# Kernel tuning notes

Hardware: AMD Instinct MI355X
Metric: run time of the kernel (lower is better)

Reference implementation:

```python
import jax, jax.numpy as jnp
import numpy as np

N = 50000          # nodes
E = 400000         # edges (before self loops)
F_IN = 128         # NUM_FEATURES
HID = 32           # hidden_dim
H = 12             # heads
HC = H * HID       # concat dim = 384
CLASSES = 40       # NUM_CLASSES
NEG_SLOPE = 0.2    # PyG GATv2 default


def setup_inputs() -> dict:
    key = jax.random.key(0)
    ks = jax.random.split(key, 16)

    def p(k, shape, fan_in):
        return (jax.random.normal(k, shape, jnp.float32) / np.sqrt(fan_in)).astype(jnp.float32)

    return {
        "x": jax.random.normal(ks[0], (N, F_IN), jnp.float32),
        "edge_index": jax.random.randint(ks[1], (2, E), 0, N, jnp.int32),
        # GATv2 layer 1 (share_weights=False)
        "Wl1": p(ks[2], (F_IN, HC), F_IN),
        "Wr1": p(ks[3], (F_IN, HC), F_IN),
        "a1": p(ks[4], (H, HID), HID),
        "b1": jnp.zeros((HC,), jnp.float32),
        # GATv2 layer 2
        "Wl2": p(ks[5], (HC, HC), HC),
        "Wr2": p(ks[6], (HC, HC), HC),
        "a2": p(ks[7], (H, HID), HID),
        "b2": jnp.zeros((HC,), jnp.float32),
        # MLP head
        "W3": p(ks[8], (HC, HID), HC),
        "b3": jnp.zeros((HID,), jnp.float32),
        "W4": p(ks[9], (HID, CLASSES), HID),
        "b4": jnp.zeros((CLASSES,), jnp.float32),
    }


def _gatv2(x, Wl, Wr, att, bias, src, dst):
    # source/target linear projections, per-head
    xl = (x @ Wl).reshape(-1, H, HID)   # [N,H,C] (message features)
    xr = (x @ Wr).reshape(-1, H, HID)   # [N,H,C]
    # per-edge attention logits: a^T LeakyReLU(xl_src + xr_dst)
    e = jax.nn.leaky_relu(xl[src] + xr[dst], NEG_SLOPE)   # [E',H,C]
    logit = jnp.einsum('ehc,hc->eh', e, att)              # [E',H]
    # segment softmax over incoming edges per dst node (self loops guarantee nonempty)
    m = jax.ops.segment_max(logit, dst, num_segments=N)   # [N,H]
    ex = jnp.exp(logit - m[dst])
    denom = jax.ops.segment_sum(ex, dst, num_segments=N)  # [N,H]
    alpha = ex / denom[dst]                                # [E',H]
    # weighted scatter-add of source messages
    out = jax.ops.segment_sum(xl[src] * alpha[:, :, None], dst, num_segments=N)
    return out.reshape(-1, HC) + bias


def reference(x, edge_index, Wl1, Wr1, a1, b1, Wl2, Wr2, a2, b2, W3, b3, W4, b4):
    # add_self_loops=True (PyG default)
    loops = jnp.arange(N, dtype=edge_index.dtype)
    src = jnp.concatenate([edge_index[0], loops])
    dst = jnp.concatenate([edge_index[1], loops])
    # dropout p=0.6 is identity in eval mode
    h = _gatv2(x, Wl1, Wr1, a1, b1, src, dst)
    h = jax.nn.elu(h)
    h = _gatv2(h, Wl2, Wr2, a2, b2, src, dst)
    h = jax.nn.elu(h)
    h = jax.nn.elu(h @ W3 + b3)
    h = h @ W4 + b4
    return jax.nn.log_softmax(h, axis=1)
```

## Files before the change

kernel.cpp:

```cpp
#include <hip/hip_runtime.h>
#include <hip/hip_bf16.h>
#include <math.h>

#define N_NODES 50000
#define E_EDGES 400000
#define EN_TOT  (E_EDGES + N_NODES)
#define F_IN    128
#define HC      384
#define CLASSES 40

typedef short short8 __attribute__((ext_vector_type(8)));
typedef float floatx4 __attribute__((ext_vector_type(4)));
typedef float floatx2 __attribute__((ext_vector_type(2)));
typedef unsigned int uint;

struct u3 { uint x, y, z; };

__device__ __forceinline__ float bf2f(unsigned short u) {
  union { unsigned int i; float f; } x; x.i = ((unsigned int)u) << 16; return x.f;
}
__device__ __forceinline__ unsigned short f2bf(float f) {
  union { float f; unsigned int i; } x; x.f = f;
  unsigned int r = x.i + 0x7fffu + ((x.i >> 16) & 1u);
  return (unsigned short)(r >> 16);
}
__device__ __forceinline__ float fin(float v) {
  return (fabsf(v) < 1e30f) ? v : 0.f;
}
__device__ __forceinline__ float rdw(const void* p, int idx, int fp32) {
  return fp32 ? ((const float*)p)[idx] : bf2f(((const unsigned short*)p)[idx]);
}

#if __has_builtin(__builtin_amdgcn_exp2f)
#define EXP2F(x) __builtin_amdgcn_exp2f(x)
#else
#define EXP2F(x) exp2f(x)
#endif

#if __has_builtin(__builtin_amdgcn_update_dpp)
#define DPP_ADD(w, ctrl) \
  (w += __int_as_float(__builtin_amdgcn_update_dpp(0, __float_as_int(w), ctrl, 0xf, 0xf, true)))
#define REDUCE16(w) do { DPP_ADD(w, 0xB1); DPP_ADD(w, 0x4E); DPP_ADD(w, 0x141); DPP_ADD(w, 0x140); } while (0)
#else
#define REDUCE16(w) do { w += __shfl_xor(w, 1); w += __shfl_xor(w, 2); \
                         w += __shfl_xor(w, 4); w += __shfl_xor(w, 8); } while (0)
#endif

__global__ void k_sentinel(float* out, int n) {
  int i = blockIdx.x * 256 + threadIdx.x;
  if (i < n) out[i] = 111.0f;
}

__global__ void k_detect_zero(const unsigned short* __restrict__ x, int* __restrict__ flag,
                              int* __restrict__ counts, int* __restrict__ cursor) {
  int i = blockIdx.x * 256 + threadIdx.x;
  if (i < N_NODES) { counts[i] = 0; cursor[i] = 0; }
  if (blockIdx.x == 0 && threadIdx.x < 64) {
    int L = threadIdx.x;
    int sane = 0;
#pragma unroll
    for (int t = 0; t < 4; ++t) {
      unsigned short u = x[(size_t)(L * 4 + t) * 2];
      unsigned int mag = u & 0x7FFFu;
      unsigned int e   = (u >> 7) & 0xFFu;
      if (mag == 0u || (e >= 96u && e <= 159u)) sane++;
    }
    sane += __shfl_xor(sane, 1);
    sane += __shfl_xor(sane, 2);
    sane += __shfl_xor(sane, 4);
    sane += __shfl_xor(sane, 8);
    sane += __shfl_xor(sane, 16);
    sane += __shfl_xor(sane, 32);
    if (L == 0) flag[0] = (sane < 179) ? 1 : 0;
  }
}

__global__ void k_cvt(const void* __restrict__ x, unsigned short* __restrict__ Xb,
                      const int* __restrict__ flagp) {
  int i = blockIdx.x * 256 + threadIdx.x;
  if (i >= N_NODES * F_IN / 8) return;
  if (flagp[0]) {
    const floatx4* p = (const floatx4*)x + (size_t)i * 2;
    floatx4 f0 = p[0], f1 = p[1];
    short8 o;
#pragma unroll
    for (int j = 0; j < 4; ++j) { o[j] = (short)f2bf(f0[j]); o[4 + j] = (short)f2bf(f1[j]); }
    ((short8*)Xb)[i] = o;
  } else {
    ((short8*)Xb)[i] = ((const short8*)x)[i];
  }
}

__global__ void k_count(const int* __restrict__ ei, int* __restrict__ counts) {
  int e = blockIdx.x * 256 + threadIdx.x;
  if (e >= EN_TOT) return;
  int dst = (e < E_EDGES) ? ei[E_EDGES + e] : (e - E_EDGES);
  if ((unsigned)dst < N_NODES) atomicAdd(&counts[dst], 1);
}

__global__ void k_scan1(const int* __restrict__ counts, int* __restrict__ row_start,
                        int* __restrict__ bsum) {
  int b = blockIdx.x, tid = threadIdx.x;
  int i = b * 1024 + tid;
  int v = (i < N_NODES) ? counts[i] : 0;
  int lane = tid & 63, w = tid >> 6;
  int x = v;
#pragma unroll
  for (int d = 1; d < 64; d <<= 1) { int t = __shfl_up(x, d); if (lane >= d) x += t; }
  __shared__ int wsum[16];
  if (lane == 63) wsum[w] = x;
  __syncthreads();
  if (w == 0) {
    int y = (lane < 16) ? wsum[lane] : 0;
#pragma unroll
    for (int d = 1; d < 16; d <<= 1) { int t = __shfl_up(y, d); if (lane >= d) y += t; }
    if (lane < 16) wsum[lane] = y;
  }
  __syncthreads();
  if (w > 0) x += wsum[w - 1];
  if (i < N_NODES) row_start[i + 1] = x;
  if (tid == 1023) bsum[b] = x;
}

__global__ void k_scan23(int* __restrict__ row_start, const int* __restrict__ bsum, int nb) {
  int b = blockIdx.x, tid = threadIdx.x;
  __shared__ int sadd;
  if (tid < 64) {
    int lane = tid;
    int x = (lane < nb) ? bsum[lane] : 0;
#pragma unroll
    for (int d = 1; d < 64; d <<= 1) { int t = __shfl_up(x, d); if (lane >= d) x += t; }
    int pre = __shfl(x, (b > 0) ? (b - 1) : 0);
    if (tid == 0) sadd = (b > 0) ? pre : 0;
  }
  __syncthreads();
  int add = sadd;
  int i = b * 1024 + tid;
  if (i < N_NODES) row_start[i + 1] += add;
  if (i == 0) row_start[0] = 0;
}

__global__ void k_fill(const int* __restrict__ ei, const int* __restrict__ row_start,
                       int* __restrict__ cursor, int* __restrict__ csr_src) {
  int e = blockIdx.x * 256 + threadIdx.x;
  if (e >= EN_TOT) return;
  int src, dst;
  if (e < E_EDGES) { src = ei[e]; dst = ei[E_EDGES + e]; }
  else             { src = dst = e - E_EDGES; }
  if ((unsigned)dst >= N_NODES) return;
  int pos = atomicAdd(&cursor[dst], 1);
  int slot = row_start[dst] + pos;
  if ((unsigned)slot < EN_TOT) csr_src[slot] = src;
}

#define PK_J1 (F_IN * HC)
#define PK_J2 (2 * PK_J1)
#define PK_J3 (PK_J2 + HC * HC)
#define PK_J4 (PK_J3 + HC * HC)
#define PK_J5 (PK_J4 + HC * 32)
__global__ void k_pack_all(const void* __restrict__ Wl1, const void* __restrict__ Wr1,
                           const void* __restrict__ Wl2, const void* __restrict__ Wr2,
                           const void* __restrict__ W3,
                           unsigned short* __restrict__ BpL1, unsigned short* __restrict__ BpR1,
                           unsigned short* __restrict__ BpL2, unsigned short* __restrict__ BpR2,
                           unsigned short* __restrict__ Bp3, const int* __restrict__ flagp) {
  int gid = blockIdx.x * 256 + threadIdx.x;
  if (gid >= PK_J5) return;
  int fp32 = flagp[0];
  const void* src; unsigned short* dst; int NT, idx;
  if (gid < PK_J2)      { NT = 24; if (gid < PK_J1) { src = Wl1; dst = BpL1; idx = gid; }
                                   else             { src = Wr1; dst = BpR1; idx = gid - PK_J1; } }
  else if (gid < PK_J4) { NT = 24; if (gid < PK_J3) { src = Wl2; dst = BpL2; idx = gid - PK_J2; }
                                   else             { src = Wr2; dst = BpR2; idx = gid - PK_J3; } }
  else                  { NT = 2;  src = W3; dst = Bp3; idx = gid - PK_J4; }
  int N  = NT * 16;
  int j  = idx & 7;
  int L  = (idx >> 3) & 63;
  int t  = idx >> 9;
  int nt = t % NT;
  int kt = t / NT;
  int k  = kt * 32 + ((L >> 4) * 8) + j;
  int n  = nt * 16 + (L & 15);
  float v = rdw(src, k * N + n, fp32);
  dst[idx] = f2bf(fin(v));
}

#define LOADB(dst, kt) do { _Pragma("unroll") for (int n = 0; n < 6; ++n) \
    dst[n] = ((const short8*)Bp)[((size_t)((kt) * 24 + nt0 + n)) * 64 + lane]; } while (0)
#define DOMFMA(bf, kt) do { \
    short8 af[4]; \
    _Pragma("unroll") for (int mf = 0; mf < 4; ++mf) { \
      int row = mf * 16 + rsel; \
      int col = (kt) * 64 + kk16 * 16; \
      af[mf] = *(const short8*)(smem + row * RS + (col ^ ((row & 7) << 4))); } \
    _Pragma("unroll") for (int n = 0; n < 6; ++n) \
      _Pragma("unroll") for (int mf = 0; mf < 4; ++mf) \
        acc[mf][n] = __builtin_amdgcn_mfma_f32_16x16x32_bf16(af[mf], bf[n], acc[mf][n], 0, 0, 0); } while (0)

template<int NK>
__global__ __launch_bounds__(256, 2) void k_gemm2(const unsigned short* __restrict__ A_,
                       const unsigned short* __restrict__ BpL,
                       const unsigned short* __restrict__ BpR,
                       unsigned short* __restrict__ CL, unsigned short* __restrict__ CR) {
  constexpr int RS = NK * 64;
  __shared__ __align__(16) char smem[64 * 776];
  int which = blockIdx.x & 1;
  int bt    = blockIdx.x >> 1;
  const unsigned short* Bp = which ? BpR : BpL;
  unsigned short* C        = which ? CR  : CL;
  int tid  = threadIdx.x;
  int wave = tid >> 6, lane = tid & 63;
  int m0   = bt * 64;

  {
    uint4 v[NK];
#pragma unroll
    for (int i = 0; i < NK; ++i) {
      int o   = (i * 256 + tid) * 16;
      int row = o / RS;
      int rem = o - row * RS;
      int rg  = m0 + row; if (rg >= N_NODES) rg = N_NODES - 1;
      v[i] = *(const uint4*)((const char*)A_ + (size_t)rg * RS + rem);
    }
#pragma unroll
    for (int i = 0; i < NK; ++i) {
      int o   = (i * 256 + tid) * 16;
      int row = o / RS;
      int rem = o - row * RS;
      *(uint4*)(smem + row * RS + (rem ^ ((row & 7) << 4))) = v[i];
    }
  }

  int nt0  = wave * 6;
  int kk16 = (lane >> 4);
  int rsel = lane & 15;
  floatx4 acc[4][6];
#pragma unroll
  for (int mf = 0; mf < 4; ++mf)
#pragma unroll
    for (int n = 0; n < 6; ++n) acc[mf][n] = (floatx4){0.f, 0.f, 0.f, 0.f};

  short8 b0[6], b1[6], b2[6];
  LOADB(b0, 0);
  LOADB(b1, 1);
  __syncthreads();

#pragma unroll
  for (int kt = 0; kt < NK; ++kt) {
    if (kt + 2 < NK) {
      if (((kt + 2) % 3) == 0)      LOADB(b0, kt + 2);
      else if (((kt + 2) % 3) == 1) LOADB(b1, kt + 2);
      else                          LOADB(b2, kt + 2);
    }
    if ((kt % 3) == 0)      DOMFMA(b0, kt);
    else if ((kt % 3) == 1) DOMFMA(b1, kt);
    else                    DOMFMA(b2, kt);
  }

  __syncthreads();
  int qr = lane >> 4, ccol = lane & 15;
#pragma unroll
  for (int n = 0; n < 6; ++n) {
    int col = (nt0 + n) * 16 + ccol;
#pragma unroll
    for (int mf = 0; mf < 4; ++mf)
#pragma unroll
      for (int r = 0; r < 4; ++r) {
        int row = mf * 16 + qr * 4 + r;
        *(unsigned short*)(smem + row * 776 + col * 2) = f2bf(fin(acc[mf][n][r]));
      }
  }
  __syncthreads();
#pragma unroll
  for (int j = 0; j < 16; ++j) {
    int row = wave * 16 + j;
    int rg  = m0 + row;
    if (rg < N_NODES) {
      u3 val = *(const u3*)(smem + row * 776 + lane * 12);
      *(u3*)((char*)C + (size_t)rg * 768 + lane * 12) = val;
    }
  }
}

__global__ void k_mlp1_mfma(const unsigned short* __restrict__ H2,
                            const unsigned short* __restrict__ Bp3,
                            const void* __restrict__ b3, float* __restrict__ H3,
                            const int* __restrict__ flagp) {
  int fp32 = flagp[0];
  int lane = threadIdx.x;
  int m0   = blockIdx.x * 16;
  int row  = m0 + (lane & 15);
  int kk   = (lane >> 4) * 8;
  floatx4 acc[2];
  acc[0] = (floatx4){0.f, 0.f, 0.f, 0.f};
  acc[1] = (floatx4){0.f, 0.f, 0.f, 0.f};
#pragma unroll
  for (int kt = 0; kt < 12; ++kt) {
    short8 af = *(const short8*)(H2 + (size_t)row * HC + kt * 32 + kk);
    const short8* bp = (const short8*)Bp3 + (size_t)kt * 2 * 64 + lane;
    acc[0] = __builtin_amdgcn_mfma_f32_16x16x32_bf16(af, bp[0],  acc[0], 0, 0, 0);
    acc[1] = __builtin_amdgcn_mfma_f32_16x16x32_bf16(af, bp[64], acc[1], 0, 0, 0);
  }
  int qr   = lane >> 4;
  int ccol = lane & 15;
#pragma unroll
  for (int nt = 0; nt < 2; ++nt)
#pragma unroll
    for (int r = 0; r < 4; ++r) {
      int col = nt * 16 + ccol;
      float s = acc[nt][r] + fin(rdw(b3, col, fp32));
      s = s > 0.f ? s : expm1f(s);
      H3[(size_t)(m0 + qr * 4 + r) * 32 + col] = fin(s);
    }
}

__global__ void k_edge(const unsigned short* __restrict__ XL, const unsigned short* __restrict__ XR,
                       const int* __restrict__ row_start, const int* __restrict__ csr_src,
                       const void* __restrict__ att, const void* __restrict__ bias,
                       unsigned short* __restrict__ H, const int* __restrict__ flagp) {
  int fp32 = flagp[0];
  int v = blockIdx.x;
  int L = threadIdx.x;
  floatx2 r2[3], a2[3];
  const uint* xr_row = (const uint*)(XR + (size_t)v * HC);
#pragma unroll
  for (int k = 0; k < 3; ++k) {
    uint rv = xr_row[L + 64 * k];
    r2[k].x = __uint_as_float(rv << 16);
    r2[k].y = __uint_as_float(rv & 0xffff0000u);
    int c = 2 * L + 128 * k;
    a2[k].x = fin(rdw(att, c,     fp32)) * 1.44269504088896f;
    a2[k].y = fin(rdw(att, c + 1, fp32)) * 1.44269504088896f;
  }
  float l[3] = {0.f, 0.f, 0.f};
  floatx2 acc[3];
#pragma unroll
  for (int k = 0; k < 3; ++k) acc[k] = (floatx2){0.f, 0.f};
  int beg = row_start[v], end = row_start[v + 1];
  if (beg < 0) beg = 0;
  if (end > EN_TOT) end = EN_TOT;
  for (int e = beg; e < end; ++e) {
    int s = csr_src[e];
    if ((unsigned)s >= N_NODES) s = 0;
    const uint* xs = (const uint*)(XL + (size_t)s * HC);
    uint qa[3];
    qa[0] = xs[L];
    qa[1] = xs[L + 64];
    qa[2] = xs[L + 128];
#pragma unroll
    for (int k = 0; k < 3; ++k) {
      floatx2 sv;
      sv.x = __uint_as_float(qa[k] << 16);
      sv.y = __uint_as_float(qa[k] & 0xffff0000u);
      floatx2 t = sv + r2[k];
      t = __builtin_elementwise_max(t, t * 0.2f);
      floatx2 dw = t * a2[k];
      float w = dw.x + dw.y;
      REDUCE16(w);
      w = fminf(fmaxf(w, -126.f), 126.f);
      float p = EXP2F(w);
      l[k] += p;
      floatx2 pv = {p, p};
      acc[k] += pv * sv;
    }
  }
  uint* hr = (uint*)(H + (size_t)v * HC);
#pragma unroll
  for (int k = 0; k < 3; ++k) {
    int c = 2 * L + 128 * k;
    float inv = 1.f / fmaxf(l[k], 1e-30f);
    float o0 = acc[k].x * inv + fin(rdw(bias, c, fp32));
    float o1 = acc[k].y * inv + fin(rdw(bias, c + 1, fp32));
    o0 = o0 > 0.f ? o0 : expm1f(o0);
    o1 = o1 > 0.f ? o1 : expm1f(o1);
    hr[L + 64 * k] = (uint)f2bf(fin(o0)) | ((uint)f2bf(fin(o1)) << 16);
  }
}

__global__ void k_mlp2(const float* __restrict__ H3, const void* __restrict__ W4,
                       const void* __restrict__ b4, float* __restrict__ out,
                       const int* __restrict__ flagp) {
  int fp32 = flagp[0];
  int v = blockIdx.x;
  int L = threadIdx.x;
  float logit = -1e30f;
  if (L < CLASSES) {
    logit = rdw(b4, L, fp32);
#pragma unroll
    for (int k = 0; k < 32; ++k)
      logit += H3[(size_t)v * 32 + k] * rdw(W4, k * CLASSES + L, fp32);
  }
  float mx = logit;
  for (int off = 1; off < 64; off <<= 1) mx = fmaxf(mx, __shfl_xor(mx, off));
  float ex = (L < CLASSES) ? __expf(logit - mx) : 0.f;
  ex = (ex == ex) ? ex : 0.f;
  float sm = ex;
  for (int off = 1; off < 64; off <<= 1) sm += __shfl_xor(sm, off);
  float ls = mx + logf(sm);
  if (L < CLASSES) out[(size_t)v * CLASSES + L] = fin(logit - ls);
}

extern "C" void kernel_launch(void* const* d_in, const int* in_sizes, int n_in,
                              void* d_out, int out_size, void* d_ws, size_t ws_size,
                              hipStream_t stream) {
  const void* x   = d_in[0];
  const int* ei   = (const int*)d_in[1];
  const void* Wl1 = d_in[2];
  const void* Wr1 = d_in[3];
  const void* a1  = d_in[4];
  const void* b1  = d_in[5];
  const void* Wl2 = d_in[6];
  const void* Wr2 = d_in[7];
  const void* a2  = d_in[8];
  const void* b2  = d_in[9];
  const void* W3  = d_in[10];
  const void* b3  = d_in[11];
  const void* W4  = d_in[12];
  const void* b4  = d_in[13];
  float* out = (float*)d_out;

  char* ws = (char*)d_ws;
  size_t off = 0;
  auto alloc = [&](size_t bytes) { size_t o = off; off += (bytes + 255) & ~(size_t)255; return o; };
  int* flag       = (int*)(ws + alloc(256));
  int* row_start  = (int*)(ws + alloc((size_t)(N_NODES + 1) * 4));
  int* counts     = (int*)(ws + alloc((size_t)N_NODES * 4));
  int* cursor     = (int*)(ws + alloc((size_t)N_NODES * 4));
  int* bsum       = (int*)(ws + alloc(64 * 4));
  int* csr_src    = (int*)(ws + alloc((size_t)EN_TOT * 4));
  unsigned short* BpL1 = (unsigned short*)(ws + alloc((size_t)F_IN * HC * 2));
  unsigned short* BpR1 = (unsigned short*)(ws + alloc((size_t)F_IN * HC * 2));
  unsigned short* BpL2 = (unsigned short*)(ws + alloc((size_t)HC * HC * 2));
  unsigned short* BpR2 = (unsigned short*)(ws + alloc((size_t)HC * HC * 2));
  unsigned short* Bp3  = (unsigned short*)(ws + alloc((size_t)HC * 32 * 2));
  unsigned short* Xb   = (unsigned short*)(ws + alloc((size_t)N_NODES * F_IN * 2));
  unsigned short* B0   = (unsigned short*)(ws + alloc((size_t)N_NODES * HC * 2));
  unsigned short* B1   = (unsigned short*)(ws + alloc((size_t)N_NODES * HC * 2));
  unsigned short* B2   = (unsigned short*)(ws + alloc((size_t)N_NODES * HC * 2));
  float* H3       = (float*)B2;
  (void)in_sizes; (void)n_in;

  if (ws_size < off) {
    k_sentinel<<<(out_size + 255) / 256, 256, 0, stream>>>(out, out_size);
    return;
  }

  const int SCAN_BLOCKS = (N_NODES + 1023) / 1024;
  const int GEMM_BLOCKS = 2 * ((N_NODES + 63) / 64);
  const int CVT_BLOCKS  = (N_NODES * F_IN / 8 + 255) / 256;

  k_detect_zero<<<(N_NODES + 255) / 256, 256, 0, stream>>>((const unsigned short*)x, flag, counts, cursor);
  k_cvt<<<CVT_BLOCKS, 256, 0, stream>>>(x, Xb, flag);
  k_count<<<(EN_TOT + 255) / 256, 256, 0, stream>>>(ei, counts);
  k_scan1<<<SCAN_BLOCKS, 1024, 0, stream>>>(counts, row_start, bsum);
  k_scan23<<<SCAN_BLOCKS, 1024, 0, stream>>>(row_start, bsum, SCAN_BLOCKS);
  k_fill<<<(EN_TOT + 255) / 256, 256, 0, stream>>>(ei, row_start, cursor, csr_src);

  k_pack_all<<<(PK_J5 + 255) / 256, 256, 0, stream>>>(Wl1, Wr1, Wl2, Wr2, W3,
                                                      BpL1, BpR1, BpL2, BpR2, Bp3, flag);

  k_gemm2<4><<<GEMM_BLOCKS, 256, 0, stream>>>(Xb, BpL1, BpR1, B0, B1);
  k_edge<<<N_NODES, 64, 0, stream>>>(B0, B1, row_start, csr_src, a1, b1, B1, flag);

  k_gemm2<12><<<GEMM_BLOCKS, 256, 0, stream>>>(B1, BpL2, BpR2, B2, B0);
  k_edge<<<N_NODES, 64, 0, stream>>>(B2, B0, row_start, csr_src, a2, b2, B1, flag);

  k_mlp1_mfma<<<N_NODES / 16, 64, 0, stream>>>(B1, Bp3, b3, H3, flag);
  k_mlp2<<<N_NODES, 64, 0, stream>>>(H3, W4, b4, out, flag);
}
```

Measured before the change: 396.7 us.

## Prefetch gathered rows in edge kernel, interleave layout, fuse MLP head with MFMA

The edge aggregation kernel now loads a batch of 64 CSR entries at once, which store precomputed byte offsets instead of source ids. It broadcasts each offset with readlane and software-prefetches the next source row while the current one is processed. The GEMM epilogue writes XL/XR in a permuted column layout so each lane fetches its three column pairs with one 12-byte load instead of three 4-byte loads. The two MLP kernels are fused into one: W4 is packed for MFMA and the log-softmax runs on DPP reductions, removing the H3 round trip and one launch. The cost is added layout coupling between the GEMM and the edge kernel, plus an extra wasted prefetch at batch ends.

```diff
diff --git a/kernel.cpp b/kernel.cpp
--- a/kernel.cpp
+++ b/kernel.cpp
@@ -41,10 +41,16 @@
 #define DPP_ADD(w, ctrl) \
   (w += __int_as_float(__builtin_amdgcn_update_dpp(0, __float_as_int(w), ctrl, 0xf, 0xf, true)))
 #define REDUCE16(w) do { DPP_ADD(w, 0xB1); DPP_ADD(w, 0x4E); DPP_ADD(w, 0x141); DPP_ADD(w, 0x140); } while (0)
+#define DPP_MAXF(w, ctrl) do { float _t = __int_as_float(__builtin_amdgcn_update_dpp(0, \
+    __float_as_int(w), ctrl, 0xf, 0xf, true)); w = fmaxf(w, _t); } while (0)
+#define RED16MAX(w) do { DPP_MAXF(w, 0xB1); DPP_MAXF(w, 0x4E); DPP_MAXF(w, 0x141); DPP_MAXF(w, 0x140); } while (0)
 #else
 #define REDUCE16(w) do { w += __shfl_xor(w, 1); w += __shfl_xor(w, 2); \
                          w += __shfl_xor(w, 4); w += __shfl_xor(w, 8); } while (0)
+#define RED16MAX(w) do { w = fmaxf(w, __shfl_xor(w, 1)); w = fmaxf(w, __shfl_xor(w, 2)); \
+                         w = fmaxf(w, __shfl_xor(w, 4)); w = fmaxf(w, __shfl_xor(w, 8)); } while (0)
 #endif
+
 
 __global__ void k_sentinel(float* out, int n) {
   int i = blockIdx.x * 256 + threadIdx.x;
@@ -141,16 +147,17 @@
 }
 
 __global__ void k_fill(const int* __restrict__ ei, const int* __restrict__ row_start,
-                       int* __restrict__ cursor, int* __restrict__ csr_src) {
+                       int* __restrict__ cursor, int* __restrict__ csr_off) {
   int e = blockIdx.x * 256 + threadIdx.x;
   if (e >= EN_TOT) return;
   int src, dst;
   if (e < E_EDGES) { src = ei[e]; dst = ei[E_EDGES + e]; }
   else             { src = dst = e - E_EDGES; }
   if ((unsigned)dst >= N_NODES) return;
+  int sv = ((unsigned)src < N_NODES) ? src : 0;
   int pos = atomicAdd(&cursor[dst], 1);
   int slot = row_start[dst] + pos;
-  if ((unsigned)slot < EN_TOT) csr_src[slot] = src;
+  if ((unsigned)slot < EN_TOT) csr_off[slot] = sv * 768;
 }
 
 #define PK_J1 (F_IN * HC)
@@ -158,22 +165,24 @@
 #define PK_J3 (PK_J2 + HC * HC)
 #define PK_J4 (PK_J3 + HC * HC)
 #define PK_J5 (PK_J4 + HC * 32)
+#define PK_J6 (PK_J5 + 32 * 48)
 __global__ void k_pack_all(const void* __restrict__ Wl1, const void* __restrict__ Wr1,
                            const void* __restrict__ Wl2, const void* __restrict__ Wr2,
-                           const void* __restrict__ W3,
+                           const void* __restrict__ W3, const void* __restrict__ W4,
                            unsigned short* __restrict__ BpL1, unsigned short* __restrict__ BpR1,
                            unsigned short* __restrict__ BpL2, unsigned short* __restrict__ BpR2,
-                           unsigned short* __restrict__ Bp3, const int* __restrict__ flagp) {
+                           unsigned short* __restrict__ Bp3, unsigned short* __restrict__ Bp4,
+                           const int* __restrict__ flagp) {
   int gid = blockIdx.x * 256 + threadIdx.x;
-  if (gid >= PK_J5) return;
+  if (gid >= PK_J6) return;
   int fp32 = flagp[0];
-  const void* src; unsigned short* dst; int NT, idx;
-  if (gid < PK_J2)      { NT = 24; if (gid < PK_J1) { src = Wl1; dst = BpL1; idx = gid; }
-                                   else             { src = Wr1; dst = BpR1; idx = gid - PK_J1; } }
-  else if (gid < PK_J4) { NT = 24; if (gid < PK_J3) { src = Wl2; dst = BpL2; idx = gid - PK_J2; }
-                                   else             { src = Wr2; dst = BpR2; idx = gid - PK_J3; } }
-  else                  { NT = 2;  src = W3; dst = Bp3; idx = gid - PK_J4; }
-  int N  = NT * 16;
+  const void* src; unsigned short* dst; int NT, NCOL, idx;
+  if (gid < PK_J2)      { NT = 24; NCOL = 384; if (gid < PK_J1) { src = Wl1; dst = BpL1; idx = gid; }
+                                               else             { src = Wr1; dst = BpR1; idx = gid - PK_J1; } }
+  else if (gid < PK_J4) { NT = 24; NCOL = 384; if (gid < PK_J3) { src = Wl2; dst = BpL2; idx = gid - PK_J2; }
+                                               else             { src = Wr2; dst = BpR2; idx = gid - PK_J3; } }
+  else if (gid < PK_J5) { NT = 2;  NCOL = 32;  src = W3; dst = Bp3; idx = gid - PK_J4; }
+  else                  { NT = 3;  NCOL = 40;  src = W4; dst = Bp4; idx = gid - PK_J5; }
   int j  = idx & 7;
   int L  = (idx >> 3) & 63;
   int t  = idx >> 9;
@@ -181,7 +190,7 @@
   int kt = t / NT;
   int k  = kt * 32 + ((L >> 4) * 8) + j;
   int n  = nt * 16 + (L & 15);
-  float v = rdw(src, k * N + n, fp32);
+  float v = (n < NCOL) ? rdw(src, k * NCOL + n, fp32) : 0.f;
   dst[idx] = f2bf(fin(v));
 }
 
@@ -261,13 +270,14 @@
   int qr = lane >> 4, ccol = lane & 15;
 #pragma unroll
   for (int n = 0; n < 6; ++n) {
-    int col = (nt0 + n) * 16 + ccol;
+    int c    = (nt0 + n) * 16 + ccol;
+    int soff = ((c & 127) >> 1) * 12 + (c >> 7) * 4 + (c & 1) * 2;
 #pragma unroll
     for (int mf = 0; mf < 4; ++mf)
 #pragma unroll
       for (int r = 0; r < 4; ++r) {
         int row = mf * 16 + qr * 4 + r;
-        *(unsigned short*)(smem + row * 776 + col * 2) = f2bf(fin(acc[mf][n][r]));
+        *(unsigned short*)(smem + row * 776 + soff) = f2bf(fin(acc[mf][n][r]));
       }
   }
   __syncthreads();
@@ -282,10 +292,83 @@
   }
 }
 
-__global__ void k_mlp1_mfma(const unsigned short* __restrict__ H2,
-                            const unsigned short* __restrict__ Bp3,
-                            const void* __restrict__ b3, float* __restrict__ H3,
-                            const int* __restrict__ flagp) {
+__global__ void k_edge(const unsigned short* __restrict__ XL, const unsigned short* __restrict__ XR,
+                       const int* __restrict__ row_start, const int* __restrict__ csr_off,
+                       const void* __restrict__ att, const void* __restrict__ bias,
+                       unsigned short* __restrict__ H, const int* __restrict__ flagp) {
+  int fp32 = flagp[0];
+  int v = blockIdx.x;
+  int L = threadIdx.x;
+  int Lo = L * 12;
+  floatx2 r2[3], a2[3];
+  u3 rv3 = *(const u3*)((const char*)XR + (size_t)v * 768 + Lo);
+  uint rr[3] = {rv3.x, rv3.y, rv3.z};
+#pragma unroll
+  for (int k = 0; k < 3; ++k) {
+    r2[k].x = __uint_as_float(rr[k] << 16);
+    r2[k].y = __uint_as_float(rr[k] & 0xffff0000u);
+    int c = 2 * L + 128 * k;
+    a2[k].x = fin(rdw(att, c,     fp32)) * 1.44269504088896f;
+    a2[k].y = fin(rdw(att, c + 1, fp32)) * 1.44269504088896f;
+  }
+  float l[3] = {0.f, 0.f, 0.f};
+  floatx2 acc[3];
+#pragma unroll
+  for (int k = 0; k < 3; ++k) acc[k] = (floatx2){0.f, 0.f};
+  int beg = row_start[v], end = row_start[v + 1];
+  if (beg < 0) beg = 0;
+  if (end > EN_TOT) end = EN_TOT;
+  const char* XLb = (const char*)XL;
+  const unsigned OMAX = (N_NODES - 1) * 768u;
+  for (int base = beg; base < end; base += 64) {
+    int nE = end - base; if (nE > 64) nE = 64;
+    int offv = (base + L < end) ? csr_off[base + L] : 0;
+    int so = __builtin_amdgcn_readlane(offv, 0);
+    if ((unsigned)so > OMAX) so = 0;
+    u3 q = *(const u3*)(XLb + (unsigned)so + Lo);
+    for (int j = 0; j < nE; ++j) {
+      int sn = __builtin_amdgcn_readlane(offv, (j + 1) & 63);
+      if ((unsigned)sn > OMAX) sn = 0;
+      u3 qn = *(const u3*)(XLb + (unsigned)sn + Lo);
+      uint qa[3] = {q.x, q.y, q.z};
+#pragma unroll
+      for (int k = 0; k < 3; ++k) {
+        floatx2 sv;
+        sv.x = __uint_as_float(qa[k] << 16);
+        sv.y = __uint_as_float(qa[k] & 0xffff0000u);
+        floatx2 t = sv + r2[k];
+        t = __builtin_elementwise_max(t, t * 0.2f);
+        floatx2 dw = t * a2[k];
+        float w = dw.x + dw.y;
+        REDUCE16(w);
+        w = fminf(fmaxf(w, -126.f), 126.f);
+        float p = EXP2F(w);
+        l[k] += p;
+        floatx2 pv = {p, p};
+        acc[k] += pv * sv;
+      }
+      q = qn;
+    }
+  }
+  uint* hr = (uint*)(H + (size_t)v * HC);
+#pragma unroll
+  for (int k = 0; k < 3; ++k) {
+    int c = 2 * L + 128 * k;
+    float inv = 1.f / fmaxf(l[k], 1e-30f);
+    float o0 = acc[k].x * inv + fin(rdw(bias, c, fp32));
+    float o1 = acc[k].y * inv + fin(rdw(bias, c + 1, fp32));
+    o0 = o0 > 0.f ? o0 : expm1f(o0);
+    o1 = o1 > 0.f ? o1 : expm1f(o1);
+    hr[L + 64 * k] = (uint)f2bf(fin(o0)) | ((uint)f2bf(fin(o1)) << 16);
+  }
+}
+
+__global__ void k_mlp(const unsigned short* __restrict__ H2,
+                      const unsigned short* __restrict__ Bp3,
+                      const unsigned short* __restrict__ Bp4,
+                      const void* __restrict__ b3, const void* __restrict__ b4,
+                      float* __restrict__ out, const int* __restrict__ flagp) {
+  __shared__ float hs[16][33];
   int fp32 = flagp[0];
   int lane = threadIdx.x;
   int m0   = blockIdx.x * 16;
@@ -301,103 +384,48 @@
     acc[0] = __builtin_amdgcn_mfma_f32_16x16x32_bf16(af, bp[0],  acc[0], 0, 0, 0);
     acc[1] = __builtin_amdgcn_mfma_f32_16x16x32_bf16(af, bp[64], acc[1], 0, 0, 0);
   }
-  int qr   = lane >> 4;
-  int ccol = lane & 15;
+  int qr = lane >> 4, cc = lane & 15;
 #pragma unroll
   for (int nt = 0; nt < 2; ++nt)
 #pragma unroll
     for (int r = 0; r < 4; ++r) {
-      int col = nt * 16 + ccol;
+      int col = nt * 16 + cc;
       float s = acc[nt][r] + fin(rdw(b3, col, fp32));
       s = s > 0.f ? s : expm1f(s);
-      H3[(size_t)(m0 + qr * 4 + r) * 32 + col] = fin(s);
-    }
-}
-
-__global__ void k_edge(const unsigned short* __restrict__ XL, const unsigned short* __restrict__ XR,
-                       const int* __restrict__ row_start, const int* __restrict__ csr_src,
-                       const void* __restrict__ att, const void* __restrict__ bias,
-                       unsigned short* __restrict__ H, const int* __restrict__ flagp) {
-  int fp32 = flagp[0];
-  int v = blockIdx.x;
-  int L = threadIdx.x;
-  floatx2 r2[3], a2[3];
-  const uint* xr_row = (const uint*)(XR + (size_t)v * HC);
-#pragma unroll
-  for (int k = 0; k < 3; ++k) {
-    uint rv = xr_row[L + 64 * k];
-    r2[k].x = __uint_as_float(rv << 16);
-    r2[k].y = __uint_as_float(rv & 0xffff0000u);
-    int c = 2 * L + 128 * k;
-    a2[k].x = fin(rdw(att, c,     fp32)) * 1.44269504088896f;
-    a2[k].y = fin(rdw(att, c + 1, fp32)) * 1.44269504088896f;
-  }
-  float l[3] = {0.f, 0.f, 0.f};
-  floatx2 acc[3];
-#pragma unroll
-  for (int k = 0; k < 3; ++k) acc[k] = (floatx2){0.f, 0.f};
-  int beg = row_start[v], end = row_start[v + 1];
-  if (beg < 0) beg = 0;
-  if (end > EN_TOT) end = EN_TOT;
-  for (int e = beg; e < end; ++e) {
-    int s = csr_src[e];
-    if ((unsigned)s >= N_NODES) s = 0;
-    const uint* xs = (const uint*)(XL + (size_t)s * HC);
-    uint qa[3];
-    qa[0] = xs[L];
-    qa[1] = xs[L + 64];
-    qa[2] = xs[L + 128];
-#pragma unroll
-    for (int k = 0; k < 3; ++k) {
-      floatx2 sv;
-      sv.x = __uint_as_float(qa[k] << 16);
-      sv.y = __uint_as_float(qa[k] & 0xffff0000u);
-      floatx2 t = sv + r2[k];
-      t = __builtin_elementwise_max(t, t * 0.2f);
-      floatx2 dw = t * a2[k];
-      float w = dw.x + dw.y;
-      REDUCE16(w);
-      w = fminf(fmaxf(w, -126.f), 126.f);
-      float p = EXP2F(w);
-      l[k] += p;
-      floatx2 pv = {p, p};
-      acc[k] += pv * sv;
-    }
-  }
-  uint* hr = (uint*)(H + (size_t)v * HC);
-#pragma unroll
-  for (int k = 0; k < 3; ++k) {
-    int c = 2 * L + 128 * k;
-    float inv = 1.f / fmaxf(l[k], 1e-30f);
-    float o0 = acc[k].x * inv + fin(rdw(bias, c, fp32));
-    float o1 = acc[k].y * inv + fin(rdw(bias, c + 1, fp32));
-    o0 = o0 > 0.f ? o0 : expm1f(o0);
-    o1 = o1 > 0.f ? o1 : expm1f(o1);
-    hr[L + 64 * k] = (uint)f2bf(fin(o0)) | ((uint)f2bf(fin(o1)) << 16);
-  }
-}
-
-__global__ void k_mlp2(const float* __restrict__ H3, const void* __restrict__ W4,
-                       const void* __restrict__ b4, float* __restrict__ out,
-                       const int* __restrict__ flagp) {
-  int fp32 = flagp[0];
-  int v = blockIdx.x;
-  int L = threadIdx.x;
-  float logit = -1e30f;
-  if (L < CLASSES) {
-    logit = rdw(b4, L, fp32);
-#pragma unroll
-    for (int k = 0; k < 32; ++k)
-      logit += H3[(size_t)v * 32 + k] * rdw(W4, k * CLASSES + L, fp32);
-  }
-  float mx = logit;
-  for (int off = 1; off < 64; off <<= 1) mx = fmaxf(mx, __shfl_xor(mx, off));
-  float ex = (L < CLASSES) ? __expf(logit - mx) : 0.f;
-  ex = (ex == ex) ? ex : 0.f;
-  float sm = ex;
-  for (int off = 1; off < 64; off <<= 1) sm += __shfl_xor(sm, off);
-  float ls = mx + logf(sm);
-  if (L < CLASSES) out[(size_t)v * CLASSES + L] = fin(logit - ls);
+      hs[qr * 4 + r][col] = fin(s);
+    }
+  __syncthreads();
+  short8 a2f;
+#pragma unroll
+  for (int j = 0; j < 8; ++j) a2f[j] = (short)f2bf(hs[lane & 15][kk + j]);
+  floatx4 lg[3];
+#pragma unroll
+  for (int nt = 0; nt < 3; ++nt) {
+    floatx4 z = (floatx4){0.f, 0.f, 0.f, 0.f};
+    lg[nt] = __builtin_amdgcn_mfma_f32_16x16x32_bf16(a2f, ((const short8*)Bp4)[nt * 64 + lane], z, 0, 0, 0);
+  }
+  float bv[3];
+#pragma unroll
+  for (int nt = 0; nt < 3; ++nt) {
+    int c = nt * 16 + cc;
+    bv[nt] = (c < CLASSES) ? fin(rdw(b4, c, fp32)) : 0.f;
+  }
+#pragma unroll
+  for (int r = 0; r < 4; ++r) {
+    float v0 = lg[0][r] + bv[0];
+    float v1 = lg[1][r] + bv[1];
+    float v2 = (cc < 8) ? (lg[2][r] + bv[2]) : -1e30f;
+    float mx = fmaxf(fmaxf(v0, v1), v2);
+    RED16MAX(mx);
+    float sm = __expf(v0 - mx) + __expf(v1 - mx) + ((cc < 8) ? __expf(v2 - mx) : 0.f);
+    sm = (sm == sm) ? sm : 1.f;
+    REDUCE16(sm);
+    float ls = mx + logf(sm);
+    float* op = out + (size_t)(m0 + qr * 4 + r) * CLASSES;
+    op[cc]      = fin(v0 - ls);
+    op[16 + cc] = fin(v1 - ls);
+    if (cc < 8) op[32 + cc] = fin(v2 - ls);
+  }
 }
 
 extern "C" void kernel_launch(void* const* d_in, const int* in_sizes, int n_in,
@@ -427,17 +455,17 @@
   int* counts     = (int*)(ws + alloc((size_t)N_NODES * 4));
   int* cursor     = (int*)(ws + alloc((size_t)N_NODES * 4));
   int* bsum       = (int*)(ws + alloc(64 * 4));
-  int* csr_src    = (int*)(ws + alloc((size_t)EN_TOT * 4));
+  int* csr_off    = (int*)(ws + alloc((size_t)EN_TOT * 4));
   unsigned short* BpL1 = (unsigned short*)(ws + alloc((size_t)F_IN * HC * 2));
   unsigned short* BpR1 = (unsigned short*)(ws + alloc((size_t)F_IN * HC * 2));
   unsigned short* BpL2 = (unsigned short*)(ws + alloc((size_t)HC * HC * 2));
   unsigned short* BpR2 = (unsigned short*)(ws + alloc((size_t)HC * HC * 2));
   unsigned short* Bp3  = (unsigned short*)(ws + alloc((size_t)HC * 32 * 2));
+  unsigned short* Bp4  = (unsigned short*)(ws + alloc((size_t)32 * 48 * 2));
   unsigned short* Xb   = (unsigned short*)(ws + alloc((size_t)N_NODES * F_IN * 2));
   unsigned short* B0   = (unsigned short*)(ws + alloc((size_t)N_NODES * HC * 2));
   unsigned short* B1   = (unsigned short*)(ws + alloc((size_t)N_NODES * HC * 2));
   unsigned short* B2   = (unsigned short*)(ws + alloc((size_t)N_NODES * HC * 2));
-  float* H3       = (float*)B2;
   (void)in_sizes; (void)n_in;
 
   if (ws_size < off) {
@@ -454,17 +482,16 @@
   k_count<<<(EN_TOT + 255) / 256, 256, 0, stream>>>(ei, counts);
   k_scan1<<<SCAN_BLOCKS, 1024, 0, stream>>>(counts, row_start, bsum);
   k_scan23<<<SCAN_BLOCKS, 1024, 0, stream>>>(row_start, bsum, SCAN_BLOCKS);
-  k_fill<<<(EN_TOT + 255) / 256, 256, 0, stream>>>(ei, row_start, cursor, csr_src);
-
-  k_pack_all<<<(PK_J5 + 255) / 256, 256, 0, stream>>>(Wl1, Wr1, Wl2, Wr2, W3,
-                                                      BpL1, BpR1, BpL2, BpR2, Bp3, flag);
+  k_fill<<<(EN_TOT + 255) / 256, 256, 0, stream>>>(ei, row_start, cursor, csr_off);
+
+  k_pack_all<<<(PK_J6 + 255) / 256, 256, 0, stream>>>(Wl1, Wr1, Wl2, Wr2, W3, W4,
+                                                      BpL1, BpR1, BpL2, BpR2, Bp3, Bp4, flag);
 
   k_gemm2<4><<<GEMM_BLOCKS, 256, 0, stream>>>(Xb, BpL1, BpR1, B0, B1);
-  k_edge<<<N_NODES, 64, 0, stream>>>(B0, B1, row_start, csr_src, a1, b1, B1, flag);
+  k_edge<<<N_NODES, 64, 0, stream>>>(B0, B1, row_start, csr_off, a1, b1, B1, flag);
 
   k_gemm2<12><<<GEMM_BLOCKS, 256, 0, stream>>>(B1, BpL2, BpR2, B2, B0);
-  k_edge<<<N_NODES, 64, 0, stream>>>(B2, B0, row_start, csr_src, a2, b2, B1, flag);
-
-  k_mlp1_mfma<<<N_NODES / 16, 64, 0, stream>>>(B1, Bp3, b3, H3, flag);
-  k_mlp2<<<N_NODES, 64, 0, stream>>>(H3, W4, b4, out, flag);
-}
+  k_edge<<<N_NODES, 64, 0, stream>>>(B2, B0, row_start, csr_off, a2, b2, B1, flag);
+
+  k_mlp<<<N_NODES / 16, 64, 0, stream>>>(B1, Bp3, Bp4, b3, b4, out, flag);
+}
```

New measurement: 381.6 us. 1.04x faster.
